# Performance work log

Measured on AMD Instinct MI355X. Metric: run time of the kernel, lower is better.

## Reference

```python
import jax, jax.numpy as jnp
import numpy as np

N, F_IN, F_OUT = 8192, 256, 128
ALPHA = 0.2  # LeakyReLU negative slope
NEG_BIG = -9e15


def setup_inputs() -> dict:
    key = jax.random.key(0)
    k1, k2, k3, k4 = jax.random.split(key, 4)
    h = jax.random.normal(k1, (N, F_IN), dtype=jnp.float32)
    adj = jax.random.randint(k2, (N, N), 0, 2, dtype=jnp.int32)
    # Xavier-uniform-ish scaled params (gain 1.414)
    w_bound = 1.414 * np.sqrt(6.0 / (F_IN + F_OUT))
    a_bound = 1.414 * np.sqrt(6.0 / (2 * F_OUT + 1))
    W = jax.random.uniform(k3, (F_IN, F_OUT), jnp.float32, -w_bound, w_bound)
    a = jax.random.uniform(k4, (2 * F_OUT, 1), jnp.float32, -a_bound, a_bound)
    return {"h": h, "adj": adj, "W": W, "a": a}


def reference(h, adj, W, a):
    # Wh: [N, F_OUT]
    Wh = h @ W
    # a = [a1; a2]; e_ij = leakyrelu(a1.Wh_i + a2.Wh_j) == the torch concat+matmul,
    # computed via broadcast-add instead of materializing [N, N, 2F].
    a1 = a[:F_OUT, 0]   # [F_OUT]
    a2 = a[F_OUT:, 0]   # [F_OUT]
    si = Wh @ a1        # [N]
    sj = Wh @ a2        # [N]
    e = jax.nn.leaky_relu(si[:, None] + sj[None, :], negative_slope=ALPHA)  # [N, N]
    logits = jnp.where(adj > 0, e, NEG_BIG)
    attention = jax.nn.softmax(logits, axis=1)
    # dropout is identity in eval mode (training=False)
    h_prime = attention @ Wh  # [N, F_OUT]
    return jax.nn.elu(h_prime)  # concat=True path
```

## Files before the change

kernel.cpp:

```cpp
#include <hip/hip_runtime.h>

#define NN 8192
#define FIN 256
#define FOUT 128
#define BKJ 128
#define JSPLIT 8
#define LALPHA 0.2f
#define NEGB -9.0e15f
#define LOG2E 1.4426950408889634f

typedef short bf16x8 __attribute__((ext_vector_type(8)));
typedef float f32x4 __attribute__((ext_vector_type(4)));

#define FOR8(X) X(0) X(1) X(2) X(3) X(4) X(5) X(6) X(7)

static __device__ __forceinline__ unsigned short f2bf(float f) {
    unsigned u = __float_as_uint(f);
    u += 0x7FFFu + ((u >> 16) & 1u);
    return (unsigned short)(u >> 16);
}
static __device__ __forceinline__ float ex2(float x) {
    float r; asm("v_exp_f32 %0, %1" : "=v"(r) : "v"(x)); return r;
}
static __device__ __forceinline__ int cvtpk(float lo, float hi) {
    int r; asm("v_cvt_pk_bf16_f32 %0, %1, %2" : "=v"(r) : "v"(lo), "v"(hi)); return r;
}

__global__ __launch_bounds__(256) void gat_k1(
    const float* __restrict__ h, const float* __restrict__ W,
    const float* __restrict__ a, unsigned short* __restrict__ WhT,
    float* __restrict__ si, float* __restrict__ sj, float* __restrict__ sjl)
{
    __shared__ float Wt[64 * 128];
    __shared__ float hT[64 * 36 + 4];
    const int t = threadIdx.x;
    const int r0 = blockIdx.x * 32;
    const int rg = t >> 5;
    const int cg = t & 31;
    float acc[4][4] = {{0.f,0.f,0.f,0.f},{0.f,0.f,0.f,0.f},{0.f,0.f,0.f,0.f},{0.f,0.f,0.f,0.f}};

    for (int kc = 0; kc < 4; ++kc) {
        __syncthreads();
        const float4* Ws = (const float4*)(W + kc * 64 * FOUT);
        float4* Wd = (float4*)Wt;
        #pragma unroll
        for (int v = 0; v < 8; ++v) Wd[v * 256 + t] = Ws[v * 256 + t];
        {
            const int hr = t >> 3, hk = (t & 7) * 8;
            const float* hs = h + (size_t)(r0 + hr) * FIN + kc * 64 + hk;
            float4 x0 = *(const float4*)hs;
            float4 x1 = *(const float4*)(hs + 4);
            hT[(hk + 0) * 36 + hr] = x0.x; hT[(hk + 1) * 36 + hr] = x0.y;
            hT[(hk + 2) * 36 + hr] = x0.z; hT[(hk + 3) * 36 + hr] = x0.w;
            hT[(hk + 4) * 36 + hr] = x1.x; hT[(hk + 5) * 36 + hr] = x1.y;
            hT[(hk + 6) * 36 + hr] = x1.z; hT[(hk + 7) * 36 + hr] = x1.w;
        }
        __syncthreads();
        #pragma unroll 8
        for (int kk = 0; kk < 64; ++kk) {
            float4 hv4 = *(const float4*)&hT[kk * 36 + rg * 4];
            float4 wv4 = *(const float4*)&Wt[kk * 128 + cg * 4];
            float hv[4] = {hv4.x, hv4.y, hv4.z, hv4.w};
            float wv[4] = {wv4.x, wv4.y, wv4.z, wv4.w};
            #pragma unroll
            for (int rr = 0; rr < 4; ++rr)
                #pragma unroll
                for (int cc = 0; cc < 4; ++cc)
                    acc[rr][cc] = fmaf(hv[rr], wv[cc], acc[rr][cc]);
        }
    }
    float4 a1v4 = *(const float4*)(a + cg * 4);
    float4 a2v4 = *(const float4*)(a + FOUT + cg * 4);
    float a1v[4] = {a1v4.x, a1v4.y, a1v4.z, a1v4.w};
    float a2v[4] = {a2v4.x, a2v4.y, a2v4.z, a2v4.w};
    float ps[4], qs[4];
    #pragma unroll
    for (int rr = 0; rr < 4; ++rr) {
        float p = 0.f, q = 0.f;
        #pragma unroll
        for (int cc = 0; cc < 4; ++cc) {
            p = fmaf(acc[rr][cc], a1v[cc], p);
            q = fmaf(acc[rr][cc], a2v[cc], q);
        }
        ps[rr] = p; qs[rr] = q;
    }
    #pragma unroll
    for (int off = 1; off <= 16; off <<= 1) {
        #pragma unroll
        for (int rr = 0; rr < 4; ++rr) {
            ps[rr] += __shfl_xor(ps[rr], off);
            qs[rr] += __shfl_xor(qs[rr], off);
        }
    }
    if (cg == 0) {
        #pragma unroll
        for (int rr = 0; rr < 4; ++rr) {
            si[r0 + rg * 4 + rr] = ps[rr];
            sj[r0 + rg * 4 + rr] = qs[rr];
            sjl[r0 + rg * 4 + rr] = qs[rr] * LOG2E;
        }
    }
    #pragma unroll
    for (int cc = 0; cc < 4; ++cc) {
        ushort4 v;
        v.x = f2bf(acc[0][cc]); v.y = f2bf(acc[1][cc]);
        v.z = f2bf(acc[2][cc]); v.w = f2bf(acc[3][cc]);
        *(ushort4*)(WhT + (size_t)(cg * 4 + cc) * NN + r0 + rg * 4) = v;
    }
}

__global__ __launch_bounds__(256) void gat_k1s(
    const float* __restrict__ sj, float* __restrict__ sjmax)
{
    __shared__ float red[256];
    float m = -1e30f;
    for (int i = threadIdx.x; i < NN; i += 256) m = fmaxf(m, sj[i]);
    red[threadIdx.x] = m;
    __syncthreads();
    for (int o = 128; o > 0; o >>= 1) {
        if (threadIdx.x < o) red[threadIdx.x] = fmaxf(red[threadIdx.x], red[threadIdx.x + o]);
        __syncthreads();
    }
    if (threadIdx.x == 0) sjmax[0] = red[0];
}

static __device__ __forceinline__ float pe(int av, float sjlv, float a2, float b2) {
    float t1 = a2 + sjlv;
    float t2 = fmaf(0.2f, sjlv, b2);
    float y = fmaxf(t1, t2);
    y = (av > 0) ? y : NEGB;
    return ex2(y);
}

template<int JS, bool FINAL>
__global__ __launch_bounds__(256, 3) void gat_k2(
    const int* __restrict__ adj, const unsigned short* __restrict__ WhT,
    const float* __restrict__ si, const float* __restrict__ sjl,
    const float* __restrict__ sjmaxp,
    float* __restrict__ lsum, float* __restrict__ Opart, float* __restrict__ out)
{
    const int JR_ = NN / JS;
    const int NST_ = JR_ / BKJ;
    __shared__ __align__(16) unsigned short tile[16384];
    const int t = threadIdx.x;
    const int w = t >> 6, l = t & 63;
    const int rb = (int)blockIdx.x / JS, js = (int)blockIdx.x % JS;
    const int iw = rb * 64 + w * 16;
    const int j0 = js * JR_;
    const int row = l & 15, kg = l >> 4;

    const float si_l = si[iw + row];
    const float sjmax = sjmaxp[0];
    const float xm = si_l + sjmax;
    const float m_row = fmaxf(xm, LALPHA * xm);
    const float a2 = (si_l - m_row) * LOG2E;
    const float b2 = (LALPHA * si_l - m_row) * LOG2E;
    const float* sjb = sjl + j0 + kg * 8;
    const int* adjb = adj + (size_t)(iw + row) * NN + j0 + kg * 8;

#define GSRC_D(v) const unsigned short* gsrc##v = WhT + (size_t)(v * 16 + (t >> 4)) * NN + j0 + (t & 15) * 8; \
                  const int ldo##v = ((v * 256 + t) * 16) ^ (((t >> 4) & 7) << 4);
    FOR8(GSRC_D)

#define REG_D(v) int4 stg##v, adr##v;
    FOR8(REG_D)
#define STG_L0(v) stg##v = *(const int4*)(gsrc##v);
    FOR8(STG_L0)
#define ADR_L0(q) adr##q = *(const int4*)(adjb + (q / 2) * 32 + (q % 2) * 4);
    FOR8(ADR_L0)

#define ACC_D(n) f32x4 acc##n = {0.f, 0.f, 0.f, 0.f};
    FOR8(ACC_D)
    f32x4 acc8 = {0.f, 0.f, 0.f, 0.f};
    bf16x8 ones;
    #pragma unroll
    for (int z = 0; z < 8; ++z) ones[z] = (short)0x3F80;
    const int kg16 = kg * 16;

#define STG_WR(v) *(int4*)((char*)tile + ldo##v) = stg##v;
#define STG_LN(v) stg##v = *(const int4*)(gsrc##v + so);
#define ADR_LN(q) adr##q = *(const int4*)(adjb + so + (q / 2) * 32 + (q % 2) * 4);
#define P8(AF, A0, A1, sp) { \
    float4 s0_ = *(const float4*)(sp); float4 s1_ = *(const float4*)((sp) + 4); \
    float p0_ = pe(A0.x, s0_.x, a2, b2), p1_ = pe(A0.y, s0_.y, a2, b2); \
    float p2_ = pe(A0.z, s0_.z, a2, b2), p3_ = pe(A0.w, s0_.w, a2, b2); \
    float p4_ = pe(A1.x, s1_.x, a2, b2), p5_ = pe(A1.y, s1_.y, a2, b2); \
    float p6_ = pe(A1.z, s1_.z, a2, b2), p7_ = pe(A1.w, s1_.w, a2, b2); \
    int4 w_; w_.x = cvtpk(p0_, p1_); w_.y = cvtpk(p2_, p3_); \
    w_.z = cvtpk(p4_, p5_); w_.w = cvtpk(p6_, p7_); \
    AF = __builtin_bit_cast(bf16x8, w_); }
#define MFMA_ROW(n) { const int c_ = n * 16 + row; \
    const int off_ = c_ * 256 + ((KB ^ ((c_ & 7) << 4))); \
    bf16x8 bv_ = *(const bf16x8*)((const char*)tile + off_); \
    acc##n = __builtin_amdgcn_mfma_f32_16x16x32_bf16(AFk, bv_, acc##n, 0, 0, 0); }
#define MFMA_KC(afv, kcl) { const bf16x8 AFk = afv; const int KB = kcl * 64 + kg16; FOR8(MFMA_ROW) \
    acc8 = __builtin_amdgcn_mfma_f32_16x16x32_bf16(AFk, ones, acc8, 0, 0, 0); }

#define BARRIER() { __builtin_amdgcn_sched_barrier(0); \
    asm volatile("s_waitcnt lgkmcnt(0)" ::: "memory"); \
    __builtin_amdgcn_s_barrier(); \
    __builtin_amdgcn_sched_barrier(0); }

    for (int s = 0; s < NST_; ++s) {
        FOR8(STG_WR)
        BARRIER()
        bf16x8 af0, af1, af2, af3;
        {
            const float* spp = sjb + s * BKJ;
            P8(af0, adr0, adr1, spp)
            P8(af1, adr2, adr3, spp + 32)
            P8(af2, adr4, adr5, spp + 64)
            P8(af3, adr6, adr7, spp + 96)
        }
        if (s + 1 < NST_) {
            const size_t so = (size_t)(s + 1) * BKJ;
            FOR8(ADR_LN)
            FOR8(STG_LN)
        }
        MFMA_KC(af0, 0) MFMA_KC(af1, 1) MFMA_KC(af2, 2) MFMA_KC(af3, 3)
        BARRIER()
    }

    if (FINAL) {
#define FN_ROW(n) { size_t ob = (size_t)(iw + kg * 4) * FOUT + n * 16 + row; \
    float o0 = acc##n[0] / acc8[0]; out[ob]            = (o0 > 0.f) ? o0 : expm1f(o0); \
    float o1 = acc##n[1] / acc8[1]; out[ob + FOUT]     = (o1 > 0.f) ? o1 : expm1f(o1); \
    float o2 = acc##n[2] / acc8[2]; out[ob + 2 * FOUT] = (o2 > 0.f) ? o2 : expm1f(o2); \
    float o3 = acc##n[3] / acc8[3]; out[ob + 3 * FOUT] = (o3 > 0.f) ? o3 : expm1f(o3); }
        FOR8(FN_ROW)
    } else {
        if (row == 0) {
            #pragma unroll
            for (int q = 0; q < 4; ++q)
                lsum[(size_t)js * NN + iw + kg * 4 + q] = acc8[q];
        }
#define ST_ROW(n) { size_t ob = ((size_t)js * NN + iw + kg * 4) * FOUT + n * 16 + row; \
    Opart[ob] = acc##n[0]; Opart[ob + FOUT] = acc##n[1]; \
    Opart[ob + 2 * FOUT] = acc##n[2]; Opart[ob + 3 * FOUT] = acc##n[3]; }
        FOR8(ST_ROW)
    }
}

__global__ __launch_bounds__(256) void gat_k3(
    const float* __restrict__ lsum, const float* __restrict__ Opart,
    float* __restrict__ out)
{
    const int t = threadIdx.x;
    const int i = (int)blockIdx.x * 2 + (t >> 7);
    const int f = t & 127;
    float den = 0.f, num = 0.f;
    const size_t SP = (size_t)NN * FOUT;
    size_t base = (size_t)i * FOUT + f;
    #pragma unroll
    for (int k = 0; k < JSPLIT; ++k) {
        den += lsum[(size_t)k * NN + i];
        num += Opart[(size_t)k * SP + base];
    }
    float o = num / den;
    out[base] = (o > 0.f) ? o : expm1f(o);
}

extern "C" void kernel_launch(void* const* d_in, const int* in_sizes, int n_in,
                              void* d_out, int out_size, void* d_ws, size_t ws_size,
                              hipStream_t stream) {
    const float* h  = (const float*)d_in[0];
    const int*  adj = (const int*)d_in[1];
    const float* W  = (const float*)d_in[2];
    const float* a  = (const float*)d_in[3];
    float* out = (float*)d_out;
    char* ws = (char*)d_ws;
    unsigned short* WhT = (unsigned short*)ws;
    float* si     = (float*)(ws + 2097152);
    float* sj     = (float*)(ws + 2129920);
    float* sjl    = (float*)(ws + 2162688);
    float* sjmax  = (float*)(ws + 2195456);
    float* lsum   = (float*)(ws + 2195712);
    float* Opart  = (float*)(ws + 2457856);
    const size_t need = 2457856 + (size_t)JSPLIT * NN * FOUT * 4;

    gat_k1<<<256, 256, 0, stream>>>(h, W, a, WhT, si, sj, sjl);
    gat_k1s<<<1, 256, 0, stream>>>(sj, sjmax);
    if (ws_size >= need) {
        gat_k2<JSPLIT, false><<<128 * JSPLIT, 256, 0, stream>>>(adj, WhT, si, sjl, sjmax, lsum, Opart, out);
        gat_k3<<<4096, 256, 0, stream>>>(lsum, Opart, out);
    } else {
        gat_k2<1, true><<<128, 256, 0, stream>>>(adj, WhT, si, sjl, sjmax, lsum, Opart, out);
    }
}
```

Baseline: 112.9 us.

## Prepack adjacency into LDS bitmask and stage sj logits in shared memory

Before the main loop, each block reads its whole adjacency slice with coalesced loads and packs it into a per-row bitmask in LDS via wave ballots. It also copies the block's slice of sj logits into LDS. The main loop then reads mask words and sj values from LDS instead of issuing per-thread int4 global loads of adj every stage, which cuts register pressure and strided global traffic. The cost is a serialized prologue with no overlap for the adjacency read, more LDS use, and a lower occupancy hint (launch bounds 3 to 2).

```diff
diff --git a/kernel.cpp b/kernel.cpp
--- a/kernel.cpp
+++ b/kernel.cpp
@@ -124,16 +124,16 @@
     if (threadIdx.x == 0) sjmax[0] = red[0];
 }
 
-static __device__ __forceinline__ float pe(int av, float sjlv, float a2, float b2) {
+static __device__ __forceinline__ float pe(unsigned bit, float sjlv, float a2, float b2) {
     float t1 = a2 + sjlv;
     float t2 = fmaf(0.2f, sjlv, b2);
     float y = fmaxf(t1, t2);
-    y = (av > 0) ? y : NEGB;
+    y = bit ? y : NEGB;
     return ex2(y);
 }
 
 template<int JS, bool FINAL>
-__global__ __launch_bounds__(256, 3) void gat_k2(
+__global__ __launch_bounds__(256, 2) void gat_k2(
     const int* __restrict__ adj, const unsigned short* __restrict__ WhT,
     const float* __restrict__ si, const float* __restrict__ sjl,
     const float* __restrict__ sjmaxp,
@@ -141,13 +141,17 @@
 {
     const int JR_ = NN / JS;
     const int NST_ = JR_ / BKJ;
+    const int MDW = JR_ / 32 + 4;
     __shared__ __align__(16) unsigned short tile[16384];
+    __shared__ __align__(16) unsigned int   mask_lds[64 * (NN / JS / 32 + 4)];
+    __shared__ __align__(16) float          sjl_lds[NN / JS];
     const int t = threadIdx.x;
     const int w = t >> 6, l = t & 63;
     const int rb = (int)blockIdx.x / JS, js = (int)blockIdx.x % JS;
     const int iw = rb * 64 + w * 16;
     const int j0 = js * JR_;
     const int row = l & 15, kg = l >> 4;
+    const int kg8 = kg * 8;
 
     const float si_l = si[iw + row];
     const float sjmax = sjmaxp[0];
@@ -155,19 +159,29 @@
     const float m_row = fmaxf(xm, LALPHA * xm);
     const float a2 = (si_l - m_row) * LOG2E;
     const float b2 = (LALPHA * si_l - m_row) * LOG2E;
-    const float* sjb = sjl + j0 + kg * 8;
-    const int* adjb = adj + (size_t)(iw + row) * NN + j0 + kg * 8;
+
+    for (int i = t * 4; i < JR_; i += 1024)
+        *(float4*)&sjl_lds[i] = *(const float4*)(sjl + j0 + i);
+
+    for (int r = 0; r < 16; ++r) {
+        const int lrow = w * 16 + r;
+        const int* arow = adj + (size_t)(rb * 64 + lrow) * NN + j0;
+        unsigned long long* mq = (unsigned long long*)&mask_lds[lrow * MDW];
+        #pragma unroll
+        for (int c = 0; c < JR_ / 64; ++c) {
+            int v = arow[c * 64 + l];
+            unsigned long long m = __ballot(v > 0);
+            if (l == 0) mq[c] = m;
+        }
+    }
 
 #define GSRC_D(v) const unsigned short* gsrc##v = WhT + (size_t)(v * 16 + (t >> 4)) * NN + j0 + (t & 15) * 8; \
                   const int ldo##v = ((v * 256 + t) * 16) ^ (((t >> 4) & 7) << 4);
     FOR8(GSRC_D)
-
-#define REG_D(v) int4 stg##v, adr##v;
+#define REG_D(v) int4 stg##v;
     FOR8(REG_D)
 #define STG_L0(v) stg##v = *(const int4*)(gsrc##v);
     FOR8(STG_L0)
-#define ADR_L0(q) adr##q = *(const int4*)(adjb + (q / 2) * 32 + (q % 2) * 4);
-    FOR8(ADR_L0)
 
 #define ACC_D(n) f32x4 acc##n = {0.f, 0.f, 0.f, 0.f};
     FOR8(ACC_D)
@@ -176,16 +190,19 @@
     #pragma unroll
     for (int z = 0; z < 8; ++z) ones[z] = (short)0x3F80;
     const int kg16 = kg * 16;
+    const unsigned int* mrow = &mask_lds[(w * 16 + row) * MDW];
+
+    __syncthreads();
 
 #define STG_WR(v) *(int4*)((char*)tile + ldo##v) = stg##v;
 #define STG_LN(v) stg##v = *(const int4*)(gsrc##v + so);
-#define ADR_LN(q) adr##q = *(const int4*)(adjb + so + (q / 2) * 32 + (q % 2) * 4);
-#define P8(AF, A0, A1, sp) { \
-    float4 s0_ = *(const float4*)(sp); float4 s1_ = *(const float4*)((sp) + 4); \
-    float p0_ = pe(A0.x, s0_.x, a2, b2), p1_ = pe(A0.y, s0_.y, a2, b2); \
-    float p2_ = pe(A0.z, s0_.z, a2, b2), p3_ = pe(A0.w, s0_.w, a2, b2); \
-    float p4_ = pe(A1.x, s1_.x, a2, b2), p5_ = pe(A1.y, s1_.y, a2, b2); \
-    float p6_ = pe(A1.z, s1_.z, a2, b2), p7_ = pe(A1.w, s1_.w, a2, b2); \
+#define P8(AF, MW, off) { \
+    float4 s0_ = *(const float4*)&sjl_lds[(off)]; float4 s1_ = *(const float4*)&sjl_lds[(off) + 4]; \
+    const unsigned sh_ = (MW) >> kg8; \
+    float p0_ = pe((sh_ >> 0) & 1u, s0_.x, a2, b2), p1_ = pe((sh_ >> 1) & 1u, s0_.y, a2, b2); \
+    float p2_ = pe((sh_ >> 2) & 1u, s0_.z, a2, b2), p3_ = pe((sh_ >> 3) & 1u, s0_.w, a2, b2); \
+    float p4_ = pe((sh_ >> 4) & 1u, s1_.x, a2, b2), p5_ = pe((sh_ >> 5) & 1u, s1_.y, a2, b2); \
+    float p6_ = pe((sh_ >> 6) & 1u, s1_.z, a2, b2), p7_ = pe((sh_ >> 7) & 1u, s1_.w, a2, b2); \
     int4 w_; w_.x = cvtpk(p0_, p1_); w_.y = cvtpk(p2_, p3_); \
     w_.z = cvtpk(p4_, p5_); w_.w = cvtpk(p6_, p7_); \
     AF = __builtin_bit_cast(bf16x8, w_); }
@@ -203,18 +220,18 @@
 
     for (int s = 0; s < NST_; ++s) {
         FOR8(STG_WR)
+        uint4 mi = *(const uint4*)(mrow + s * 4);
         BARRIER()
         bf16x8 af0, af1, af2, af3;
         {
-            const float* spp = sjb + s * BKJ;
-            P8(af0, adr0, adr1, spp)
-            P8(af1, adr2, adr3, spp + 32)
-            P8(af2, adr4, adr5, spp + 64)
-            P8(af3, adr6, adr7, spp + 96)
+            const int off = s * BKJ + kg8;
+            P8(af0, mi.x, off)
+            P8(af1, mi.y, off + 32)
+            P8(af2, mi.z, off + 64)
+            P8(af3, mi.w, off + 96)
         }
         if (s + 1 < NST_) {
             const size_t so = (size_t)(s + 1) * BKJ;
-            FOR8(ADR_LN)
             FOR8(STG_LN)
         }
         MFMA_KC(af0, 0) MFMA_KC(af1, 1) MFMA_KC(af2, 2) MFMA_KC(af3, 3)
```

After: 307.1 us. 2.72x slower.
